# Kernel optimization log

Measured on AMD Instinct MI355X. Metric: run time of the kernel, lower is better.

The kernel has to match this reference:

```python
import jax, jax.numpy as jnp
import numpy as np

B, C, Cs, CI, H, W = 4, 256, 256, 128, 64, 64

def setup_inputs() -> dict:
    key = jax.random.key(0)
    ks = jax.random.split(key, 9)
    sq = 1.0 / np.sqrt(C)
    ss = 1.0 / np.sqrt(Cs)
    return {
        "x_main": jax.random.normal(ks[0], (B, C, H, W), jnp.float32),
        "z_p": jax.random.normal(ks[1], (B, Cs, H, W), jnp.float32),
        "Wq": jax.random.normal(ks[2], (CI, C), jnp.float32) * sq,
        "bq": jax.random.normal(ks[3], (CI,), jnp.float32) * 0.01,
        "Wk": jax.random.normal(ks[4], (CI, Cs), jnp.float32) * ss,
        "bk": jax.random.normal(ks[5], (CI,), jnp.float32) * 0.01,
        "Wv": jax.random.normal(ks[6], (C, Cs), jnp.float32) * ss,
        "bv": jax.random.normal(ks[7], (C,), jnp.float32) * 0.01,
        "gamma": jax.random.normal(ks[8], (1,), jnp.float32) * 0.1,
    }

def reference(x_main, z_p, Wq, bq, Wk, bk, Wv, bv, gamma):
    b, c, h, w = x_main.shape
    n = h * w
    xm = x_main.reshape(b, c, n)          # [B, C, N]
    zf = z_p.reshape(b, z_p.shape[1], n)  # [B, Cs, M] (M == N here)
    # 1x1 convs == per-pixel channel projections
    q = jnp.einsum('oc,bcn->bon', Wq, xm) + bq[None, :, None]  # [B, CI, N]
    k = jnp.einsum('oc,bcm->bom', Wk, zf) + bk[None, :, None]  # [B, CI, M]
    v = jnp.einsum('oc,bcm->bom', Wv, zf) + bv[None, :, None]  # [B, C, M]
    # energy[b, n, m] = q_n . k_m  (no scaling, as in the original)
    energy = jnp.einsum('bcn,bcm->bnm', q, k)
    attention = jax.nn.softmax(energy, axis=-1)
    out = jnp.einsum('bom,bnm->bon', v, attention)  # [B, C, N]
    out = out.reshape(b, c, h, w)
    return gamma * out + x_main
```

## Files before the change

kernel.cpp:

```cpp
#include <hip/hip_runtime.h>
#include <hip/hip_bf16.h>


typedef __bf16  bf16x8  __attribute__((ext_vector_type(8)));
typedef float   f32x16  __attribute__((ext_vector_type(16)));

#define LOG2E 1.4426950408889634f

union BF8 { __hip_bfloat162 h[4]; bf16x8 v; };
union U4  { unsigned u[4]; bf16x8 v; };

__device__ inline bf16x8 pack8(const float f[8]) {
  BF8 u;
#pragma unroll
  for (int i = 0; i < 4; i++)
    u.h[i] = __float22bfloat162_rn(float2{f[2 * i], f[2 * i + 1]});
  return u.v;
}

__device__ inline void dma16(const void* g, void* l) {
  __builtin_amdgcn_global_load_lds(
      (const __attribute__((address_space(1))) unsigned int*)g,
      (__attribute__((address_space(3))) unsigned int*)l, 16, 0, 0);
}

__global__ __launch_bounds__(256) void wprep_kernel(
    const float* __restrict__ Wq, const float* __restrict__ Wk,
    const float* __restrict__ Wv, __hip_bfloat16* __restrict__ wfr)
{
  const int base = blockIdx.x * 1024;
  const int tid = threadIdx.x;
#pragma unroll
  for (int i = 0; i < 4; i++) {
    int c = base + i * 256 + tid;
    const float* Ws; __hip_bfloat16* dst; int rc;
    if (c < 4096)      { Ws = Wq; dst = wfr;          rc = c; }
    else if (c < 8192) { Ws = Wk; dst = wfr + 32768;  rc = c - 4096; }
    else               { Ws = Wv; dst = wfr + 65536;  rc = c - 8192; }
    int ot = rc >> 10, cs = (rc >> 6) & 15, rem = rc & 63;
    int hf = rem >> 5, l32 = rem & 31;
    const float* src = Ws + (ot * 32 + l32) * 256 + cs * 16 + hf * 8;
    float f[8];
#pragma unroll
    for (int j = 0; j < 8; j++) f[j] = src[j];
    *(bf16x8*)(dst + ot * 8192 + cs * 512 + hf * 256 + l32 * 8) = pack8(f);
  }
}

struct PFSmem {
  float stg[128 * 68];
  alignas(16) __hip_bfloat16 frag[16384];
};

__global__ __launch_bounds__(512, 2) void projfused(
    const float* __restrict__ x, const float* __restrict__ z,
    const __hip_bfloat16* __restrict__ wfr,
    const float* __restrict__ bq, const float* __restrict__ bk,
    const float* __restrict__ bv,
    __hip_bfloat16* __restrict__ qp, __hip_bfloat16* __restrict__ kp,
    __hip_bfloat16* __restrict__ vp)
{
  __shared__ PFSmem sm;
  const int bi = blockIdx.x;
  const bool qmode = bi < 256;
  const int j2 = qmode ? bi : bi - 256;
  const int b = j2 >> 6, pc = j2 & 63;
  const float* in = qmode ? x : z;
  const size_t ib = (size_t)b * 256 * 4096 + pc * 64;

  const int tid = threadIdx.x, w = tid >> 6, lane = tid & 63,
            l32 = lane & 31, half = lane >> 5;
  const int pix4 = (tid & 15) * 4;

#pragma unroll
  for (int it = 0; it < 4; it++) {
    int ch = it * 32 + (tid >> 4);
    float4 v4 = *(const float4*)&in[ib + (size_t)ch * 4096 + pix4];
    *(float4*)&sm.stg[ch * 68 + pix4] = v4;
  }
  __syncthreads();
#pragma unroll
  for (int i = 0; i < 2; i++) {
    int c = i * 512 + tid;
    int grp = c >> 9, csl = (c >> 6) & 7, rem = c & 63;
    int hf = rem >> 5, lr = rem & 31;
    int chb = csl * 16 + hf * 8;
    float f[8];
#pragma unroll
    for (int j = 0; j < 8; j++) f[j] = sm.stg[(chb + j) * 68 + grp * 32 + lr];
    *(bf16x8*)(sm.frag + grp * 8192 + csl * 512 + hf * 256 + lr * 8) = pack8(f);
  }
  __syncthreads();

#pragma unroll
  for (int it = 0; it < 4; it++) {
    int ch = it * 32 + (tid >> 4);
    float4 v4 = *(const float4*)&in[ib + (size_t)(128 + ch) * 4096 + pix4];
    *(float4*)&sm.stg[ch * 68 + pix4] = v4;
  }
  __syncthreads();
#pragma unroll
  for (int i = 0; i < 2; i++) {
    int c = i * 512 + tid;
    int grp = c >> 9, csl = (c >> 6) & 7, rem = c & 63;
    int hf = rem >> 5, lr = rem & 31;
    int chb = csl * 16 + hf * 8;
    float f[8];
#pragma unroll
    for (int j = 0; j < 8; j++) f[j] = sm.stg[(chb + j) * 68 + grp * 32 + lr];
    *(bf16x8*)(sm.frag + grp * 8192 + (csl + 8) * 512 + hf * 256 + lr * 8) =
        pack8(f);
  }
  __syncthreads();

  const int t4 = (l32 >> 2) & 3;
  const int kperm = (t4 == 1 || t4 == 2) ? (l32 ^ 12) : l32;

  if (qmode) {
    const int ot = w >> 1, pg = w & 1;
    bf16x8 bfr[16];
#pragma unroll
    for (int cs = 0; cs < 16; cs++)
      bfr[cs] = *(const bf16x8*)(sm.frag + pg * 8192 + cs * 512 + lane * 8);
    const __hip_bfloat16* wp = wfr + ot * 8192 + lane * 8;
    bf16x8 wfg[16];
#pragma unroll
    for (int cs = 0; cs < 16; cs++) wfg[cs] = *(const bf16x8*)(wp + cs * 512);
    float bb[16];
#pragma unroll
    for (int r = 0; r < 16; r++)
      bb[r] = bq[ot * 32 + (r & 3) + 8 * (r >> 2) + 4 * half];
    f32x16 O = {};
#pragma unroll
    for (int cs = 0; cs < 16; cs++)
      O = __builtin_amdgcn_mfma_f32_32x32x16_bf16(wfg[cs], bfr[cs], O, 0, 0, 0);
    __hip_bfloat16* qb = qp + ((size_t)(b * 128 + pc * 2 + pg)) * 4096;
#pragma unroll
    for (int r = 0; r < 16; r++) {
      int oc = ot * 32 + (r & 3) + 8 * (r >> 2) + 4 * half;
      qb[(oc >> 4) * 512 + ((oc >> 3) & 1) * 256 + l32 * 8 + (oc & 7)] =
          __float2bfloat16((O[r] + bb[r]) * LOG2E);
    }
  } else {
    const int pg = w & 1;
    bf16x8 bfr[16];
#pragma unroll
    for (int cs = 0; cs < 16; cs++)
      bfr[cs] = *(const bf16x8*)(sm.frag + pg * 8192 + cs * 512 + lane * 8);
    const size_t pgg = (size_t)(b * 128 + pc * 2 + pg);
#pragma unroll
    for (int jj = 0; jj < 3; jj++) {
      const int t = (w + jj * 8) >> 1;
      const bool isK = (t < 4);
      const __hip_bfloat16* wp = wfr + (isK ? 32768 + t * 8192
                                            : 65536 + (t - 4) * 8192) + lane * 8;
      bf16x8 wfg[16];
#pragma unroll
      for (int cs = 0; cs < 16; cs++) wfg[cs] = *(const bf16x8*)(wp + cs * 512);
      const float* bias = isK ? bk : bv;
      const int ocb = (isK ? t : t - 4) * 32;
      float bb[16];
#pragma unroll
      for (int r = 0; r < 16; r++)
        bb[r] = bias[ocb + (r & 3) + 8 * (r >> 2) + 4 * half];
      f32x16 O = {};
#pragma unroll
      for (int cs = 0; cs < 16; cs++)
        O = __builtin_amdgcn_mfma_f32_32x32x16_bf16(wfg[cs], bfr[cs], O, 0, 0, 0);
      if (isK) {
        __hip_bfloat16* kb = kp + pgg * 4096;
#pragma unroll
        for (int r = 0; r < 16; r++) {
          int oc = t * 32 + (r & 3) + 8 * (r >> 2) + 4 * half;
          kb[(oc >> 4) * 512 + ((oc >> 3) & 1) * 256 + kperm * 8 + (oc & 7)] =
              __float2bfloat16(O[r] + bb[r]);
        }
      } else {
        __hip_bfloat16* vb = vp + pgg * 8192 + (t - 4) * 1024
            + (l32 >> 4) * 512 + ((l32 >> 3) & 1) * 256 + (l32 & 7);
#pragma unroll
        for (int r = 0; r < 16; r++) {
          int rr = (r & 3) + 8 * (r >> 2) + 4 * half;
          vb[rr * 8] = __float2bfloat16(O[r] + bb[r]);
        }
      }
    }
  }
}

struct AttnSmem {
  union {
    struct {
      __hip_bfloat16 kbuf[3][8192];
      __hip_bfloat16 qlds[8192];
    } m;
    float ostage[256][65];
  } u;
  float redu[4][64];
  float rinv[64];
};

__global__ __launch_bounds__(256, 1) void attn_kernel(
    const __hip_bfloat16* __restrict__ qv, const __hip_bfloat16* __restrict__ kv,
    const __hip_bfloat16* __restrict__ vv,
    const float* __restrict__ x_main, const float* __restrict__ gammap,
    float* __restrict__ out)
{
  __shared__ AttnSmem sm;
  const int i   = blockIdx.x;
  const int b   = (i & 7) >> 1;
  const int qt2 = ((i >> 3) << 1) | (i & 1);
  const int qtA = qt2 * 2;
  const int n0  = qt2 * 64;
  const int tid = threadIdx.x;
  const int w   = tid >> 6, lane = tid & 63, l32 = lane & 31;
  const int kh  = w >> 1, chh = w & 1;
  const int t0  = qt2 & 63;

  {
    const __hip_bfloat16* qsrc = qv + ((size_t)(b * 128 + qtA)) * 4096;
#pragma unroll
    for (int j = 0; j < 4; j++)
      *(bf16x8*)(sm.u.m.qlds + j * 2048 + tid * 8) =
          *(const bf16x8*)(qsrc + j * 2048 + tid * 8);
  }

  const __hip_bfloat16* kg = kv + (size_t)(b * 128) * 4096;
  const __hip_bfloat16* vg = vv + (size_t)(b * 128) * 8192;

  auto stage = [&](int ta, int par) {
    __hip_bfloat16* kd = sm.u.m.kbuf[par];
    const __hip_bfloat16* ksrc = kg + (size_t)ta * 8192 + lane * 8;
#pragma unroll
    for (int c = 0; c < 4; c++) {
      int ck = w * 4 + c;
      dma16(ksrc + ck * 512, kd + ck * 512 + lane * 8);
    }
  };

  f32x16 OA[4], OB[4];
#pragma unroll
  for (int c = 0; c < 4; c++)
#pragma unroll
    for (int r = 0; r < 16; r++) { OA[c][r] = 0.f; OB[c][r] = 0.f; }

  float lA = 0.f, lB = 0.f;

  auto softmax = [&](const f32x16& S, bf16x8& pf0, bf16x8& pf1, float& lacc) {
    unsigned p2[8];
    float lsub = 0.f;
#pragma unroll
    for (int i2 = 0; i2 < 8; i2++) {
      float a = exp2f(S[2 * i2]     - 64.0f);
      float c = exp2f(S[2 * i2 + 1] - 64.0f);
      lsub += a + c;
      union { __hip_bfloat162 h; unsigned u; } cv;
      cv.h = __float22bfloat162_rn(float2{a, c});
      p2[i2] = cv.u;
    }
    lacc += lsub;
    U4 f0, f1;
    f0.u[0] = p2[0]; f0.u[1] = p2[1]; f0.u[2] = p2[2]; f0.u[3] = p2[3];
    f1.u[0] = p2[4]; f1.u[1] = p2[5]; f1.u[2] = p2[6]; f1.u[3] = p2[7];
    pf0 = f0.v; pf1 = f1.v;
  };

  stage(t0, 0);
  stage((t0 + 1) & 63, 1);
  __syncthreads();

#pragma unroll 1
  for (int lt = 0; lt < 64; ++lt) {
    const int ta = (lt + t0) & 63;

    const __hip_bfloat16* vb = vg + (size_t)(ta * 2 + kh) * 8192
                             + chh * 4096 + lane * 8;
    bf16x8 Vc[8];
#pragma unroll
    for (int c = 0; c < 4; c++) {
      Vc[2 * c]     = *(const bf16x8*)(vb + c * 1024);
      Vc[2 * c + 1] = *(const bf16x8*)(vb + c * 1024 + 512);
    }
    __builtin_amdgcn_sched_barrier(0);

    if (lt < 62) stage((lt + 2 + t0) & 63, (lt + 2) % 3);

    const __hip_bfloat16* kbase = sm.u.m.kbuf[lt % 3] + kh * 4096 + lane * 8;
    const __hip_bfloat16* qab   = sm.u.m.qlds + lane * 8;
    f32x16 SA = {}, SB = {};
#pragma unroll
    for (int cs = 0; cs < 8; cs++) {
      bf16x8 kf = *(const bf16x8*)(kbase + cs * 512);
      bf16x8 qa = *(const bf16x8*)(qab + cs * 512);
      bf16x8 qb2 = *(const bf16x8*)(qab + 4096 + cs * 512);
      SA = __builtin_amdgcn_mfma_f32_32x32x16_bf16(kf, qa,  SA, 0, 0, 0);
      SB = __builtin_amdgcn_mfma_f32_32x32x16_bf16(kf, qb2, SB, 0, 0, 0);
    }

    bf16x8 pf0, pf1;
    softmax(SA, pf0, pf1, lA);
#pragma unroll
    for (int c = 0; c < 4; c++) {
      OA[c] = __builtin_amdgcn_mfma_f32_32x32x16_bf16(Vc[2 * c],     pf0, OA[c], 0, 0, 0);
      OA[c] = __builtin_amdgcn_mfma_f32_32x32x16_bf16(Vc[2 * c + 1], pf1, OA[c], 0, 0, 0);
    }
    softmax(SB, pf0, pf1, lB);
#pragma unroll
    for (int c = 0; c < 4; c++) {
      OB[c] = __builtin_amdgcn_mfma_f32_32x32x16_bf16(Vc[2 * c],     pf0, OB[c], 0, 0, 0);
      OB[c] = __builtin_amdgcn_mfma_f32_32x32x16_bf16(Vc[2 * c + 1], pf1, OB[c], 0, 0, 0);
    }

    if (lt < 63) {
      __builtin_amdgcn_sched_barrier(0);
      __builtin_amdgcn_s_barrier();
      __builtin_amdgcn_sched_barrier(0);
    }
  }

  float lfA = lA + __shfl_xor(lA, 32);
  float lfB = lB + __shfl_xor(lB, 32);
  if (lane < 32) { sm.redu[w][l32] = lfA; sm.redu[w][32 + l32] = lfB; }
  __syncthreads();
  const int hb = lane >> 5;
  if (kh == 0) {
#pragma unroll
    for (int c = 0; c < 4; c++) {
#pragma unroll
      for (int r = 0; r < 16; r++) {
        int ch = (chh * 4 + c) * 32 + (r & 3) + 8 * (r >> 2) + 4 * hb;
        sm.u.ostage[ch][l32]      = OA[c][r];
        sm.u.ostage[ch][32 + l32] = OB[c][r];
      }
    }
  }
  if (tid < 64) sm.rinv[tid] = 1.0f / (sm.redu[0][tid] + sm.redu[2][tid]);
  __syncthreads();
  if (kh == 1) {
#pragma unroll
    for (int c = 0; c < 4; c++) {
#pragma unroll
      for (int r = 0; r < 16; r++) {
        int ch = (chh * 4 + c) * 32 + (r & 3) + 8 * (r >> 2) + 4 * hb;
        sm.u.ostage[ch][l32]      += OA[c][r];
        sm.u.ostage[ch][32 + l32] += OB[c][r];
      }
    }
  }
  __syncthreads();

  const float gmm = gammap[0];
  const int pix = tid & 63;
  const float ri = sm.rinv[pix];
#pragma unroll 1
  for (int j = 0; j < 64; ++j) {
    int ch = j * 4 + (tid >> 6);
    size_t g = ((size_t)(b * 256 + ch)) * 4096 + n0 + pix;
    out[g] = gmm * sm.u.ostage[ch][pix] * ri + x_main[g];
  }
}

extern "C" void kernel_launch(void* const* d_in, const int* in_sizes, int n_in,
                              void* d_out, int out_size, void* d_ws, size_t ws_size,
                              hipStream_t stream) {
  (void)in_sizes; (void)n_in; (void)out_size; (void)ws_size;
  const float* x  = (const float*)d_in[0];
  const float* z  = (const float*)d_in[1];
  const float* Wq = (const float*)d_in[2];
  const float* bq = (const float*)d_in[3];
  const float* Wk = (const float*)d_in[4];
  const float* bk = (const float*)d_in[5];
  const float* Wv = (const float*)d_in[6];
  const float* bv = (const float*)d_in[7];
  const float* gm = (const float*)d_in[8];
  float* out = (float*)d_out;

  char* ws = (char*)d_ws;
  const size_t MB = 1024 * 1024;
  __hip_bfloat16* qp  = (__hip_bfloat16*)(ws);
  __hip_bfloat16* kp  = (__hip_bfloat16*)(ws + 4 * MB);
  __hip_bfloat16* vp  = (__hip_bfloat16*)(ws + 8 * MB);
  __hip_bfloat16* wfp = (__hip_bfloat16*)(ws + 16 * MB);

  wprep_kernel<<<16, 256, 0, stream>>>(Wq, Wk, Wv, wfp);
  projfused   <<<512, 512, 0, stream>>>(x, z, wfp, bq, bk, bv, qp, kp, vp);
  attn_kernel <<<256, 256, 0, stream>>>(qp, kp, vp, x, gm, out);
}
```

Baseline: 227.3 us.

## Split attention over key halves with merge kernel; fold weight prep into projection

```diff
diff --git a/kernel.cpp b/kernel.cpp
--- a/kernel.cpp
+++ b/kernel.cpp
@@ -24,37 +24,27 @@
       (__attribute__((address_space(3))) unsigned int*)l, 16, 0, 0);
 }
 
-__global__ __launch_bounds__(256) void wprep_kernel(
-    const float* __restrict__ Wq, const float* __restrict__ Wk,
-    const float* __restrict__ Wv, __hip_bfloat16* __restrict__ wfr)
-{
-  const int base = blockIdx.x * 1024;
-  const int tid = threadIdx.x;
-#pragma unroll
-  for (int i = 0; i < 4; i++) {
-    int c = base + i * 256 + tid;
-    const float* Ws; __hip_bfloat16* dst; int rc;
-    if (c < 4096)      { Ws = Wq; dst = wfr;          rc = c; }
-    else if (c < 8192) { Ws = Wk; dst = wfr + 32768;  rc = c - 4096; }
-    else               { Ws = Wv; dst = wfr + 65536;  rc = c - 8192; }
-    int ot = rc >> 10, cs = (rc >> 6) & 15, rem = rc & 63;
-    int hf = rem >> 5, l32 = rem & 31;
-    const float* src = Ws + (ot * 32 + l32) * 256 + cs * 16 + hf * 8;
-    float f[8];
-#pragma unroll
-    for (int j = 0; j < 8; j++) f[j] = src[j];
-    *(bf16x8*)(dst + ot * 8192 + cs * 512 + hf * 256 + l32 * 8) = pack8(f);
-  }
-}
-
 struct PFSmem {
   float stg[128 * 68];
   alignas(16) __hip_bfloat16 frag[16384];
 };
 
+__device__ inline void wload(const float* Ws, int ot, int l32, int half,
+                             bf16x8* wfg) {
+  const float* wsrc = Ws + (ot * 32 + l32) * 256 + half * 8;
+#pragma unroll
+  for (int cs = 0; cs < 16; cs++) {
+    float f[8];
+#pragma unroll
+    for (int j = 0; j < 8; j++) f[j] = wsrc[cs * 16 + j];
+    wfg[cs] = pack8(f);
+  }
+}
+
 __global__ __launch_bounds__(512, 2) void projfused(
     const float* __restrict__ x, const float* __restrict__ z,
-    const __hip_bfloat16* __restrict__ wfr,
+    const float* __restrict__ Wq, const float* __restrict__ Wk,
+    const float* __restrict__ Wv,
     const float* __restrict__ bq, const float* __restrict__ bk,
     const float* __restrict__ bv,
     __hip_bfloat16* __restrict__ qp, __hip_bfloat16* __restrict__ kp,
@@ -122,10 +112,8 @@
 #pragma unroll
     for (int cs = 0; cs < 16; cs++)
       bfr[cs] = *(const bf16x8*)(sm.frag + pg * 8192 + cs * 512 + lane * 8);
-    const __hip_bfloat16* wp = wfr + ot * 8192 + lane * 8;
     bf16x8 wfg[16];
-#pragma unroll
-    for (int cs = 0; cs < 16; cs++) wfg[cs] = *(const bf16x8*)(wp + cs * 512);
+    wload(Wq, ot, l32, half, wfg);
     float bb[16];
 #pragma unroll
     for (int r = 0; r < 16; r++)
@@ -152,17 +140,14 @@
     for (int jj = 0; jj < 3; jj++) {
       const int t = (w + jj * 8) >> 1;
       const bool isK = (t < 4);
-      const __hip_bfloat16* wp = wfr + (isK ? 32768 + t * 8192
-                                            : 65536 + (t - 4) * 8192) + lane * 8;
+      const int tt = isK ? t : t - 4;
       bf16x8 wfg[16];
-#pragma unroll
-      for (int cs = 0; cs < 16; cs++) wfg[cs] = *(const bf16x8*)(wp + cs * 512);
+      wload(isK ? Wk : Wv, tt, l32, half, wfg);
       const float* bias = isK ? bk : bv;
-      const int ocb = (isK ? t : t - 4) * 32;
       float bb[16];
 #pragma unroll
       for (int r = 0; r < 16; r++)
-        bb[r] = bias[ocb + (r & 3) + 8 * (r >> 2) + 4 * half];
+        bb[r] = bias[tt * 32 + (r & 3) + 8 * (r >> 2) + 4 * half];
       f32x16 O = {};
 #pragma unroll
       for (int cs = 0; cs < 16; cs++)
@@ -176,7 +161,7 @@
               __float2bfloat16(O[r] + bb[r]);
         }
       } else {
-        __hip_bfloat16* vb = vp + pgg * 8192 + (t - 4) * 1024
+        __hip_bfloat16* vb = vp + pgg * 8192 + tt * 1024
             + (l32 >> 4) * 512 + ((l32 >> 3) & 1) * 256 + (l32 & 7);
 #pragma unroll
         for (int r = 0; r < 16; r++) {
@@ -200,22 +185,28 @@
   float rinv[64];
 };
 
-__global__ __launch_bounds__(256, 1) void attn_kernel(
+template <int SPLIT>
+__global__ __launch_bounds__(256, 2) void attn_kernel(
     const __hip_bfloat16* __restrict__ qv, const __hip_bfloat16* __restrict__ kv,
     const __hip_bfloat16* __restrict__ vv,
     const float* __restrict__ x_main, const float* __restrict__ gammap,
-    float* __restrict__ out)
+    float* __restrict__ out,
+    float* __restrict__ part, float* __restrict__ lpart)
 {
   __shared__ AttnSmem sm;
   const int i   = blockIdx.x;
   const int b   = (i & 7) >> 1;
-  const int qt2 = ((i >> 3) << 1) | (i & 1);
+  int qt2, kt2;
+  if (SPLIT) { int j = i >> 3; kt2 = j >> 5; qt2 = ((j & 31) << 1) | (i & 1); }
+  else       { kt2 = 0;        qt2 = ((i >> 3) << 1) | (i & 1); }
+  const int NT = SPLIT ? 32 : 64;
+  const int sbase = SPLIT ? kt2 * 32 : 0;
   const int qtA = qt2 * 2;
   const int n0  = qt2 * 64;
   const int tid = threadIdx.x;
   const int w   = tid >> 6, lane = tid & 63, l32 = lane & 31;
   const int kh  = w >> 1, chh = w & 1;
-  const int t0  = qt2 & 63;
+  const int t0  = qt2 & (NT - 1);
 
   {
     const __hip_bfloat16* qsrc = qv + ((size_t)(b * 128 + qtA)) * 4096;
@@ -228,9 +219,9 @@
   const __hip_bfloat16* kg = kv + (size_t)(b * 128) * 4096;
   const __hip_bfloat16* vg = vv + (size_t)(b * 128) * 8192;
 
-  auto stage = [&](int ta, int par) {
+  auto stage = [&](int tl, int par) {
     __hip_bfloat16* kd = sm.u.m.kbuf[par];
-    const __hip_bfloat16* ksrc = kg + (size_t)ta * 8192 + lane * 8;
+    const __hip_bfloat16* ksrc = kg + (size_t)(sbase + tl) * 8192 + lane * 8;
 #pragma unroll
     for (int c = 0; c < 4; c++) {
       int ck = w * 4 + c;
@@ -266,12 +257,12 @@
   };
 
   stage(t0, 0);
-  stage((t0 + 1) & 63, 1);
+  stage((t0 + 1) & (NT - 1), 1);
   __syncthreads();
 
 #pragma unroll 1
-  for (int lt = 0; lt < 64; ++lt) {
-    const int ta = (lt + t0) & 63;
+  for (int lt = 0; lt < NT; ++lt) {
+    const int ta = sbase + ((lt + t0) & (NT - 1));
 
     const __hip_bfloat16* vb = vg + (size_t)(ta * 2 + kh) * 8192
                              + chh * 4096 + lane * 8;
@@ -283,15 +274,15 @@
     }
     __builtin_amdgcn_sched_barrier(0);
 
-    if (lt < 62) stage((lt + 2 + t0) & 63, (lt + 2) % 3);
+    if (lt < NT - 2) stage((lt + 2 + t0) & (NT - 1), (lt + 2) % 3);
 
     const __hip_bfloat16* kbase = sm.u.m.kbuf[lt % 3] + kh * 4096 + lane * 8;
     const __hip_bfloat16* qab   = sm.u.m.qlds + lane * 8;
     f32x16 SA = {}, SB = {};
 #pragma unroll
     for (int cs = 0; cs < 8; cs++) {
-      bf16x8 kf = *(const bf16x8*)(kbase + cs * 512);
-      bf16x8 qa = *(const bf16x8*)(qab + cs * 512);
+      bf16x8 kf  = *(const bf16x8*)(kbase + cs * 512);
+      bf16x8 qa  = *(const bf16x8*)(qab + cs * 512);
       bf16x8 qb2 = *(const bf16x8*)(qab + 4096 + cs * 512);
       SA = __builtin_amdgcn_mfma_f32_32x32x16_bf16(kf, qa,  SA, 0, 0, 0);
       SB = __builtin_amdgcn_mfma_f32_32x32x16_bf16(kf, qb2, SB, 0, 0, 0);
@@ -311,7 +302,7 @@
       OB[c] = __builtin_amdgcn_mfma_f32_32x32x16_bf16(Vc[2 * c + 1], pf1, OB[c], 0, 0, 0);
     }
 
-    if (lt < 63) {
+    if (lt < NT - 1) {
       __builtin_amdgcn_sched_barrier(0);
       __builtin_amdgcn_s_barrier();
       __builtin_amdgcn_sched_barrier(0);
@@ -334,7 +325,9 @@
       }
     }
   }
-  if (tid < 64) sm.rinv[tid] = 1.0f / (sm.redu[0][tid] + sm.redu[2][tid]);
+  if (!SPLIT) {
+    if (tid < 64) sm.rinv[tid] = 1.0f / (sm.redu[0][tid] + sm.redu[2][tid]);
+  }
   __syncthreads();
   if (kh == 1) {
 #pragma unroll
@@ -349,21 +342,54 @@
   }
   __syncthreads();
 
-  const float gmm = gammap[0];
-  const int pix = tid & 63;
-  const float ri = sm.rinv[pix];
+  if (SPLIT) {
+    const int pblk = (b * 64 + qt2) * 2 + kt2;
+    if (tid < 64)
+      lpart[(size_t)pblk * 64 + tid] = sm.redu[0][tid] + sm.redu[2][tid];
+    float* pb = part + (size_t)pblk * 16384;
+#pragma unroll 4
+    for (int j = 0; j < 64; ++j) {
+      int idx = j * 256 + tid;
+      pb[idx] = sm.u.ostage[idx >> 6][idx & 63];
+    }
+  } else {
+    const float gmm = gammap[0];
+    const int pix = tid & 63;
+    const float ri = sm.rinv[pix];
 #pragma unroll 1
+    for (int j = 0; j < 64; ++j) {
+      int ch = j * 4 + (tid >> 6);
+      size_t g = ((size_t)(b * 256 + ch)) * 4096 + n0 + pix;
+      out[g] = gmm * sm.u.ostage[ch][pix] * ri + x_main[g];
+    }
+  }
+}
+
+__global__ __launch_bounds__(256) void merge_kernel(
+    const float* __restrict__ part, const float* __restrict__ lpart,
+    const float* __restrict__ x_main, const float* __restrict__ gammap,
+    float* __restrict__ out)
+{
+  const int i = blockIdx.x;
+  const int b = i >> 6, qt2 = i & 63, n0 = qt2 * 64;
+  const int tid = threadIdx.x, pix = tid & 63;
+  const size_t pb = (size_t)((b * 64 + qt2) * 2) * 16384;
+  const float* lp = lpart + (size_t)((b * 64 + qt2) * 2) * 64;
+  const float rv = gammap[0] / (lp[pix] + lp[64 + pix]);
+#pragma unroll 4
   for (int j = 0; j < 64; ++j) {
-    int ch = j * 4 + (tid >> 6);
+    int idx = j * 256 + tid;
+    int ch = idx >> 6;
     size_t g = ((size_t)(b * 256 + ch)) * 4096 + n0 + pix;
-    out[g] = gmm * sm.u.ostage[ch][pix] * ri + x_main[g];
+    float o = (part[pb + idx] + part[pb + 16384 + idx]) * rv;
+    out[g] = o + x_main[g];
   }
 }
 
 extern "C" void kernel_launch(void* const* d_in, const int* in_sizes, int n_in,
                               void* d_out, int out_size, void* d_ws, size_t ws_size,
                               hipStream_t stream) {
-  (void)in_sizes; (void)n_in; (void)out_size; (void)ws_size;
+  (void)in_sizes; (void)n_in; (void)out_size;
   const float* x  = (const float*)d_in[0];
   const float* z  = (const float*)d_in[1];
   const float* Wq = (const float*)d_in[2];
@@ -380,9 +406,16 @@
   __hip_bfloat16* qp  = (__hip_bfloat16*)(ws);
   __hip_bfloat16* kp  = (__hip_bfloat16*)(ws + 4 * MB);
   __hip_bfloat16* vp  = (__hip_bfloat16*)(ws + 8 * MB);
-  __hip_bfloat16* wfp = (__hip_bfloat16*)(ws + 16 * MB);
-
-  wprep_kernel<<<16, 256, 0, stream>>>(Wq, Wk, Wv, wfp);
-  projfused   <<<512, 512, 0, stream>>>(x, z, wfp, bq, bk, bv, qp, kp, vp);
-  attn_kernel <<<256, 256, 0, stream>>>(qp, kp, vp, x, gm, out);
-}
+  float* part  = (float*)(ws + 16 * MB);
+  float* lpart = (float*)(ws + 48 * MB);
+
+  const bool split = ws_size >= 49 * MB;
+
+  projfused<<<512, 512, 0, stream>>>(x, z, Wq, Wk, Wv, bq, bk, bv, qp, kp, vp);
+  if (split) {
+    attn_kernel<1><<<512, 256, 0, stream>>>(qp, kp, vp, x, gm, out, part, lpart);
+    merge_kernel<<<256, 256, 0, stream>>>(part, lpart, x, gm, out);
+  } else {
+    attn_kernel<0><<<256, 256, 0, stream>>>(qp, kp, vp, x, gm, out, part, lpart);
+  }
+}
```

Measured after the change: 224.5 us. Within noise of the previous version (-1.2%).
